# Optimization experiments

Measured on AMD Instinct MI355X. Metric: run time of the kernel, lower is better.

## Reference

```python
import jax, jax.numpy as jnp
import numpy as np

DROPOUT_RATE = 0.6


def dropout(x, key, rate=DROPOUT_RATE):
    keep = jax.random.bernoulli(key, 1.0 - rate, x.shape)
    return jnp.where(keep, x / (1.0 - rate), 0.0).astype(x.dtype)


def gcn_conv(x, W, b, src, dst, n_nodes):
    # h = x @ W  (tiny linear), then symmetric-normalized scatter-add over edges
    h = x @ W                                             # [N, C_out]
    deg = jax.ops.segment_sum(jnp.ones_like(dst, dtype=h.dtype), dst,
                              num_segments=n_nodes)       # in-degree at targets
    dinv = jnp.where(deg > 0, jax.lax.rsqrt(jnp.maximum(deg, 1.0)), 0.0)
    norm = dinv[src] * dinv[dst]                          # [E]
    msg = h[src] * norm[:, None]                          # [E, C_out] gather
    out = jax.ops.segment_sum(msg, dst, num_segments=n_nodes)  # scatter-add
    return out + b


def setup_inputs() -> dict:
    key = jax.random.key(0)
    k_x, k_e, k_w1, k_w2 = jax.random.split(key, 4)
    N, E = 100000, 6400000
    x = jax.random.normal(k_x, (N, 1), dtype=jnp.float32)
    edge_index = jax.random.randint(k_e, (2, E), 0, N, dtype=jnp.int64)
    # GCNConv weights (glorot-ish scale) and zero biases
    W1 = jax.random.normal(k_w1, (1, 16), dtype=jnp.float32) * (1.0 / np.sqrt(1.0))
    b1 = jnp.zeros((16,), dtype=jnp.float32)
    W2 = jax.random.normal(k_w2, (16, 1), dtype=jnp.float32) * (1.0 / np.sqrt(16.0))
    b2 = jnp.zeros((1,), dtype=jnp.float32)
    return {"x": x, "edge_index": edge_index, "W1": W1, "b1": b1, "W2": W2, "b2": b2}


def reference(x, edge_index, W1, b1, W2, b2):
    n_nodes = x.shape[0]
    src, dst = edge_index[0], edge_index[1]
    k1, k2 = jax.random.split(jax.random.key(42), 2)
    h = dropout(x, k1)
    h = gcn_conv(h, W1, b1, src, dst, n_nodes)
    h = jax.nn.relu(h)
    h = dropout(h, k2)
    out = gcn_conv(h, W2, b2, src, dst, n_nodes)
    return out
```

## Files before the change

kernel.cpp:

```cpp
#include <hip/hip_runtime.h>
#include <hip/hip_bf16.h>
#include <stdint.h>


#define KEEP_P 0.4f
#define RANGE 2048
#define SHIFT 11
#define MASK 2047
#define QRANGE 8192
#define QSHIFT 13
#define QMASK 8191
#define BPC 512
#define NCELLMAX 1024
#define TILE 8192
#define TILE4 (TILE / 4)

__host__ __device__ inline unsigned rotl32(unsigned v, int s) {
  return (v << s) | (v >> (32 - s));
}

__host__ __device__ inline void threefry2x32(unsigned key0, unsigned key1,
                                             unsigned x0, unsigned x1,
                                             unsigned& o0, unsigned& o1) {
  unsigned ks0 = key0, ks1 = key1, ks2 = key0 ^ key1 ^ 0x1BD11BDAu;
  unsigned v0 = x0 + ks0, v1 = x1 + ks1;
#define TF_R(r) { v0 += v1; v1 = rotl32(v1, r); v1 ^= v0; }
  TF_R(13) TF_R(15) TF_R(26) TF_R(6)
  v0 += ks1; v1 += ks2 + 1u;
  TF_R(17) TF_R(29) TF_R(16) TF_R(24)
  v0 += ks2; v1 += ks0 + 2u;
  TF_R(13) TF_R(15) TF_R(26) TF_R(6)
  v0 += ks0; v1 += ks1 + 3u;
  TF_R(17) TF_R(29) TF_R(16) TF_R(24)
  v0 += ks1; v1 += ks2 + 4u;
  TF_R(13) TF_R(15) TF_R(26) TF_R(6)
  v0 += ks2; v1 += ks0 + 5u;
#undef TF_R
  o0 = v0; o1 = v1;
}

__device__ inline float u01_from_bits(unsigned bits) {
  return __uint_as_float((bits >> 9) | 0x3f800000u) - 1.0f;
}

__global__ __launch_bounds__(256) void k_cnt(
    const int* __restrict__ src, const int* __restrict__ dst,
    unsigned* __restrict__ counts, int NCELL, int NQ, int e4, int E) {
  __shared__ unsigned cnt[NCELLMAX];
  const int tid = threadIdx.x;
  for (int c = tid; c < NCELL; c += 256) cnt[c] = 0u;
  __syncthreads();
  const int chunk = (e4 + BPC - 1) / BPC;
  const int j0 = blockIdx.x * chunk, j1 = min(j0 + chunk, e4);
  const int4* d4 = reinterpret_cast<const int4*>(dst);
  const int4* s4 = reinterpret_cast<const int4*>(src);
#define CNT1(d, s) atomicAdd(&cnt[((unsigned)(d) >> SHIFT) * NQ + \
                                  ((unsigned)(s) >> QSHIFT)], 1u);
  for (int j = j0 + tid; j < j1; j += 256) {
    int4 d = d4[j]; int4 s = s4[j];
    CNT1(d.x, s.x) CNT1(d.y, s.y) CNT1(d.z, s.z) CNT1(d.w, s.w)
  }
  if (blockIdx.x == 0) {
    for (int t = e4 * 4 + tid; t < E; t += 256) CNT1(dst[t], src[t])
  }
#undef CNT1
  __syncthreads();
  unsigned* my = counts + (size_t)blockIdx.x * NCELL;
  for (int c = tid; c < NCELL; c += 256) my[c] = cnt[c];
}

__global__ __launch_bounds__(256) void k_scan1(
    const unsigned* __restrict__ counts, unsigned* __restrict__ bases,
    unsigned* __restrict__ total, int NCELL) {
  __shared__ unsigned sc[256];
  const int c = blockIdx.x, t = threadIdx.x;
  unsigned c0 = counts[(size_t)(2 * t) * NCELL + c];
  unsigned c1 = counts[(size_t)(2 * t + 1) * NCELL + c];
  unsigned s = c0 + c1;
  sc[t] = s;
  __syncthreads();
  for (int ofs = 1; ofs < 256; ofs <<= 1) {
    unsigned v = (t >= ofs) ? sc[t - ofs] : 0u;
    __syncthreads();
    sc[t] += v;
    __syncthreads();
  }
  unsigned excl = sc[t] - s;
  bases[(size_t)(2 * t) * NCELL + c] = excl;
  bases[(size_t)(2 * t + 1) * NCELL + c] = excl + c0;
  if (t == 255) total[c] = sc[255];
}

__global__ __launch_bounds__(256) void k_scan2(
    const unsigned* __restrict__ total, unsigned* __restrict__ cellstart,
    int NCELL, int E) {
  __shared__ unsigned sc[256];
  const int t = threadIdx.x;
  unsigned l[4]; unsigned s = 0;
  for (int k = 0; k < 4; ++k) {
    int idx = t * 4 + k;
    unsigned v = (idx < NCELL) ? total[idx] : 0u;
    l[k] = s; s += v;
  }
  sc[t] = s;
  __syncthreads();
  for (int ofs = 1; ofs < 256; ofs <<= 1) {
    unsigned v = (t >= ofs) ? sc[t - ofs] : 0u;
    __syncthreads();
    sc[t] += v;
    __syncthreads();
  }
  unsigned excl = sc[t] - s;
  for (int k = 0; k < 4; ++k) {
    int idx = t * 4 + k;
    if (idx < NCELL) cellstart[idx] = excl + l[k];
  }
  if (t == 255) cellstart[NCELL] = (unsigned)E;
}

__global__ __launch_bounds__(256) void k_part(
    const int* __restrict__ src, const int* __restrict__ dst,
    const unsigned* __restrict__ bases, const unsigned* __restrict__ cellstart,
    unsigned* __restrict__ rec, int NCELL, int NQ, int e4, int E) {
  __shared__ unsigned stage[TILE];
  __shared__ unsigned short cellid[TILE];
  __shared__ unsigned hist[NCELLMAX], off[NCELLMAX], tscan[NCELLMAX];
  __shared__ unsigned tbase[NCELLMAX], blkcur[NCELLMAX];
  __shared__ unsigned ssum[256];
  const int tid = threadIdx.x;
  const unsigned* myb = bases + (size_t)blockIdx.x * NCELL;
  for (int c = tid; c < NCELL; c += 256) blkcur[c] = cellstart[c] + myb[c];
  const int chunk = (e4 + BPC - 1) / BPC;
  const int j0 = blockIdx.x * chunk, j1 = min(j0 + chunk, e4);
  const int4* d4 = reinterpret_cast<const int4*>(dst);
  const int4* s4 = reinterpret_cast<const int4*>(src);
  const int K = (NCELL + 255) / 256;

  for (int t0 = j0; t0 < j1; t0 += TILE4) {
    __syncthreads();
    for (int c = tid; c < NCELL; c += 256) hist[c] = 0u;
    __syncthreads();
    const int tcnt = min(TILE4, j1 - t0);
    for (int jj = tid; jj < tcnt; jj += 256) {
      int4 d = d4[t0 + jj]; int4 s = s4[t0 + jj];
      atomicAdd(&hist[((unsigned)d.x >> SHIFT) * NQ + ((unsigned)s.x >> QSHIFT)], 1u);
      atomicAdd(&hist[((unsigned)d.y >> SHIFT) * NQ + ((unsigned)s.y >> QSHIFT)], 1u);
      atomicAdd(&hist[((unsigned)d.z >> SHIFT) * NQ + ((unsigned)s.z >> QSHIFT)], 1u);
      atomicAdd(&hist[((unsigned)d.w >> SHIFT) * NQ + ((unsigned)s.w >> QSHIFT)], 1u);
    }
    __syncthreads();
    unsigned l[4]; unsigned s = 0;
    for (int k = 0; k < K; ++k) {
      int c = tid * K + k;
      unsigned v = (c < NCELL) ? hist[c] : 0u;
      l[k] = s; s += v;
    }
    ssum[tid] = s;
    __syncthreads();
    for (int ofs = 1; ofs < 256; ofs <<= 1) {
      unsigned v = (tid >= ofs) ? ssum[tid - ofs] : 0u;
      __syncthreads();
      ssum[tid] += v;
      __syncthreads();
    }
    unsigned excl = ssum[tid] - s;
    for (int k = 0; k < K; ++k) {
      int c = tid * K + k;
      if (c < NCELL) {
        unsigned e = excl + l[k];
        off[c] = e; tscan[c] = e;
        tbase[c] = blkcur[c];
        blkcur[c] += hist[c];
      }
    }
    __syncthreads();
    for (int jj = tid; jj < tcnt; jj += 256) {
      int4 d = d4[t0 + jj]; int4 s2 = s4[t0 + jj];
#define STG1(dd, ss) { unsigned ud = (unsigned)(dd), us = (unsigned)(ss); \
      unsigned cell = (ud >> SHIFT) * NQ + (us >> QSHIFT); \
      unsigned pos = atomicAdd(&off[cell], 1u); \
      stage[pos] = (ud & MASK) | ((us & QMASK) << SHIFT); \
      cellid[pos] = (unsigned short)cell; }
      STG1(d.x, s2.x) STG1(d.y, s2.y) STG1(d.z, s2.z) STG1(d.w, s2.w)
#undef STG1
    }
    __syncthreads();
    const int tc = 4 * tcnt;
    for (int i = tid; i < tc; i += 256) {
      unsigned c = cellid[i];
      rec[tbase[c] + ((unsigned)i - tscan[c])] = stage[i];
    }
  }
  __syncthreads();
  if (blockIdx.x == 0) {
    for (int t = e4 * 4 + tid; t < E; t += 256) {
      unsigned ud = (unsigned)dst[t], us = (unsigned)src[t];
      unsigned cell = (ud >> SHIFT) * NQ + (us >> QSHIFT);
      unsigned pos = atomicAdd(&blkcur[cell], 1u);
      rec[pos] = (ud & MASK) | ((us & QMASK) << SHIFT);
    }
  }
}

__global__ __launch_bounds__(256) void k_deg(
    const unsigned* __restrict__ rec, const unsigned* __restrict__ cellstart,
    unsigned short* __restrict__ degpart, int NB, int NQ, int SJ) {
  __shared__ unsigned bins[RANGE / 2];
  const int tid = threadIdx.x;
  const int j = blockIdx.x, p = blockIdx.y;
  for (int i = tid; i < RANGE / 2; i += 256) bins[i] = 0u;
  __syncthreads();
  const int s0 = (int)cellstart[p * NQ], s1 = (int)cellstart[(p + 1) * NQ];
  const int len = s1 - s0;
  const int a = s0 + (int)((long)len * j / SJ);
  const int b = s0 + (int)((long)len * (j + 1) / SJ);
#define DEG1(v) { unsigned r = (v) & MASK; \
    atomicAdd(&bins[r >> 1], 1u << ((r & 1) * 16)); }
  int i = a + tid;
  for (; i + 768 < b; i += 1024) {
    unsigned v0 = rec[i], v1 = rec[i + 256], v2 = rec[i + 512], v3 = rec[i + 768];
    DEG1(v0) DEG1(v1) DEG1(v2) DEG1(v3)
  }
  for (; i < b; i += 256) DEG1(rec[i])
#undef DEG1
  __syncthreads();
  unsigned* my32 = (unsigned*)(degpart + ((size_t)j * NB + p) * RANGE);
  for (int i2 = tid; i2 < RANGE / 2; i2 += 256) my32[i2] = bins[i2];
}

__global__ __launch_bounds__(256) void k_node1(
    const float* __restrict__ x, const unsigned short* __restrict__ degpart,
    float* __restrict__ dinv, float* __restrict__ y,
    int NB, int SJ, int n, unsigned k1a, unsigned k1b) {
  int i = blockIdx.x * blockDim.x + threadIdx.x;
  if (i >= n) return;
  const int p = i >> SHIFT, r = i & MASK;
  unsigned d = 0;
  for (int j = 0; j < SJ; ++j) d += degpart[((size_t)j * NB + p) * RANGE + r];
  float di = (d > 0) ? (1.0f / sqrtf((float)d)) : 0.0f;
  dinv[i] = di;
  unsigned o0, o1;
  threefry2x32(k1a, k1b, 0u, (unsigned)i, o0, o1);
  float u = u01_from_bits(o0 ^ o1);
  float xd = (u < KEEP_P) ? (x[i] / KEEP_P) : 0.0f;
  y[i] = xd * di;
}

__global__ __launch_bounds__(256) void k_scat(
    const unsigned* __restrict__ rec, const unsigned* __restrict__ cellstart,
    const float* __restrict__ val, float* __restrict__ part,
    int NB, int NQ, int N) {
  __shared__ float cache[QRANGE];
  __shared__ float bins[RANGE];
  const int tid = threadIdx.x;
  const int q = blockIdx.x, p = blockIdx.y;
  const int g0 = q * QRANGE;
  const int lim = min(QRANGE, N - g0);
  for (int i = tid; i < lim; i += 256) cache[i] = val[g0 + i];
  for (int i = tid; i < RANGE; i += 256) bins[i] = 0.0f;
  __syncthreads();
  const int s0 = (int)cellstart[p * NQ + q], s1 = (int)cellstart[p * NQ + q + 1];
  int i = s0 + tid;
  for (; i + 768 < s1; i += 1024) {
    unsigned v0 = rec[i], v1 = rec[i + 256], v2 = rec[i + 512], v3 = rec[i + 768];
    float f0 = cache[v0 >> SHIFT], f1 = cache[v1 >> SHIFT];
    float f2 = cache[v2 >> SHIFT], f3 = cache[v3 >> SHIFT];
    atomicAdd(&bins[v0 & MASK], f0);
    atomicAdd(&bins[v1 & MASK], f1);
    atomicAdd(&bins[v2 & MASK], f2);
    atomicAdd(&bins[v3 & MASK], f3);
  }
  for (; i < s1; i += 256) {
    unsigned v = rec[i];
    atomicAdd(&bins[v & MASK], cache[v >> SHIFT]);
  }
  __syncthreads();
  float* my = part + ((size_t)q * NB + p) * RANGE;
  for (int i2 = tid; i2 < RANGE; i2 += 256) my[i2] = bins[i2];
}

__global__ __launch_bounds__(256) void k_node2(
    const float* __restrict__ part, const float* __restrict__ dinv,
    const float* __restrict__ W1, const float* __restrict__ b1,
    const float* __restrict__ W2, float* __restrict__ z2,
    int NB, int NQ, int n, unsigned k2a, unsigned k2b) {
  int i = blockIdx.x * blockDim.x + threadIdx.x;
  if (i >= n) return;
  const int p = i >> SHIFT, r = i & MASK;
  float s = 0.0f;
  for (int q = 0; q < NQ; ++q) s += part[((size_t)q * NB + p) * RANGE + r];
  float t = s * dinv[i];
  float z = 0.0f;
  unsigned base = (unsigned)i * 16u;
#pragma unroll
  for (int c = 0; c < 16; ++c) {
    float h = W1[c] * t + b1[c];
    h = fmaxf(h, 0.0f);
    unsigned o0, o1;
    threefry2x32(k2a, k2b, 0u, base + (unsigned)c, o0, o1);
    float u = u01_from_bits(o0 ^ o1);
    float hd = (u < KEEP_P) ? (h / KEEP_P) : 0.0f;
    z += hd * W2[c];
  }
  z2[i] = z * dinv[i];
}

__global__ __launch_bounds__(256) void k_final(
    const float* __restrict__ part, const float* __restrict__ dinv,
    const float* __restrict__ b2, float* __restrict__ out,
    int NB, int NQ, int n) {
  int i = blockIdx.x * blockDim.x + threadIdx.x;
  if (i >= n) return;
  const int p = i >> SHIFT, r = i & MASK;
  float s = 0.0f;
  for (int q = 0; q < NQ; ++q) s += part[((size_t)q * NB + p) * RANGE + r];
  out[i] = b2[0] + dinv[i] * s;
}

extern "C" void kernel_launch(void* const* d_in, const int* in_sizes, int n_in,
                              void* d_out, int out_size, void* d_ws, size_t ws_size,
                              hipStream_t stream) {
  const float* x  = (const float*)d_in[0];
  const int* edge = (const int*)d_in[1];
  const float* W1 = (const float*)d_in[2];
  const float* b1 = (const float*)d_in[3];
  const float* W2 = (const float*)d_in[4];
  const float* b2 = (const float*)d_in[5];
  float* out = (float*)d_out;

  const int N = in_sizes[0];
  const int E = in_sizes[1] / 2;
  const int* src = edge;
  const int* dst = edge + E;

  const int NP = (N + 255) & ~255;
  const int NB = (N + RANGE - 1) / RANGE;
  const int NQ = (N + QRANGE - 1) / QRANGE;
  const int NCELL = NB * NQ;
  const int DSJ = 2 * NQ;

  char* w = (char*)d_ws;
  auto align256 = [](char* p) {
    return (char*)(((uintptr_t)p + 255) & ~(uintptr_t)255);
  };
  unsigned* counts = (unsigned*)w;  w = align256(w + (size_t)BPC * NCELL * 4);
  unsigned* bases  = (unsigned*)w;  w = align256(w + (size_t)BPC * NCELL * 4);
  unsigned* total  = (unsigned*)w;  w = align256(w + (size_t)NCELL * 4);
  unsigned* cellst = (unsigned*)w;  w = align256(w + (size_t)(NCELL + 1) * 4);
  unsigned* rec    = (unsigned*)w;  w = align256(w + (size_t)E * 4);
  float* part_f = (float*)w;
  unsigned short* degpart = (unsigned short*)w;
  size_t part_bytes = (size_t)NQ * NB * RANGE * 4;
  size_t deg_bytes  = (size_t)DSJ * NB * RANGE * 2;
  w = align256(w + (part_bytes > deg_bytes ? part_bytes : deg_bytes));
  float* dinv = (float*)w;
  float* y    = dinv + NP;
  float* z2   = y + NP;

  unsigned k1a, k1b, k2a, k2b;
  threefry2x32(0u, 42u, 0u, 0u, k1a, k1b);
  threefry2x32(0u, 42u, 0u, 1u, k2a, k2b);

  const int e4 = E >> 2;
  const int gN = (N + 255) / 256;

  k_cnt  <<<BPC, 256, 0, stream>>>(src, dst, counts, NCELL, NQ, e4, E);
  k_scan1<<<NCELL, 256, 0, stream>>>(counts, bases, total, NCELL);
  k_scan2<<<1, 256, 0, stream>>>(total, cellst, NCELL, E);
  k_part <<<BPC, 256, 0, stream>>>(src, dst, bases, cellst, rec, NCELL, NQ, e4, E);
  k_deg  <<<dim3(DSJ, NB), 256, 0, stream>>>(rec, cellst, degpart, NB, NQ, DSJ);
  k_node1<<<gN, 256, 0, stream>>>(x, degpart, dinv, y, NB, DSJ, N, k1a, k1b);
  k_scat <<<dim3(NQ, NB), 256, 0, stream>>>(rec, cellst, y, part_f, NB, NQ, N);
  k_node2<<<gN, 256, 0, stream>>>(part_f, dinv, W1, b1, W2, z2, NB, NQ, N, k2a, k2b);
  k_scat <<<dim3(NQ, NB), 256, 0, stream>>>(rec, cellst, z2, part_f, NB, NQ, N);
  k_final<<<gN, 256, 0, stream>>>(part_f, dinv, b2, out, NB, NQ, N);
}
```

Baseline: 260.2 us.

## Decouple count and partition grid sizes, async LDS cache fill, deeper unroll

Splits the single blocks-per-chunk constant into a larger grid for the counting pass and a smaller one for the partition pass, so each partition block takes the combined range of several count blocks. The scan now sums several count entries per thread. The scatter kernel fills its value cache with direct global-to-LDS loads, and both the scatter and degree loops are unrolled to eight loads per iteration for more memory-level parallelism. Costs include a larger counts/bases workspace, longer per-block work in the partition pass, and more register pressure from the wider unroll.

New measurement: 276.2 us. 1.06x slower.

```diff
diff --git a/kernel.cpp b/kernel.cpp
--- a/kernel.cpp
+++ b/kernel.cpp
@@ -10,7 +10,9 @@
 #define QRANGE 8192
 #define QSHIFT 13
 #define QMASK 8191
-#define BPC 512
+#define BPCC 2048
+#define BPCP 256
+#define RATIO (BPCC / BPCP)
 #define NCELLMAX 1024
 #define TILE 8192
 #define TILE4 (TILE / 4)
@@ -50,7 +52,7 @@
   const int tid = threadIdx.x;
   for (int c = tid; c < NCELL; c += 256) cnt[c] = 0u;
   __syncthreads();
-  const int chunk = (e4 + BPC - 1) / BPC;
+  const int chunk = (e4 + BPCC - 1) / BPCC;
   const int j0 = blockIdx.x * chunk, j1 = min(j0 + chunk, e4);
   const int4* d4 = reinterpret_cast<const int4*>(dst);
   const int4* s4 = reinterpret_cast<const int4*>(src);
@@ -74,9 +76,12 @@
     unsigned* __restrict__ total, int NCELL) {
   __shared__ unsigned sc[256];
   const int c = blockIdx.x, t = threadIdx.x;
-  unsigned c0 = counts[(size_t)(2 * t) * NCELL + c];
-  unsigned c1 = counts[(size_t)(2 * t + 1) * NCELL + c];
-  unsigned s = c0 + c1;
+  unsigned l[RATIO];
+  unsigned s = 0;
+  for (int k = 0; k < RATIO; ++k) {
+    unsigned v = counts[(size_t)(t * RATIO + k) * NCELL + c];
+    l[k] = s; s += v;
+  }
   sc[t] = s;
   __syncthreads();
   for (int ofs = 1; ofs < 256; ofs <<= 1) {
@@ -86,8 +91,8 @@
     __syncthreads();
   }
   unsigned excl = sc[t] - s;
-  bases[(size_t)(2 * t) * NCELL + c] = excl;
-  bases[(size_t)(2 * t + 1) * NCELL + c] = excl + c0;
+  for (int k = 0; k < RATIO; ++k)
+    bases[(size_t)(t * RATIO + k) * NCELL + c] = excl + l[k];
   if (t == 255) total[c] = sc[255];
 }
 
@@ -128,9 +133,10 @@
   __shared__ unsigned tbase[NCELLMAX], blkcur[NCELLMAX];
   __shared__ unsigned ssum[256];
   const int tid = threadIdx.x;
-  const unsigned* myb = bases + (size_t)blockIdx.x * NCELL;
+  const unsigned* myb = bases + (size_t)blockIdx.x * RATIO * NCELL;
   for (int c = tid; c < NCELL; c += 256) blkcur[c] = cellstart[c] + myb[c];
-  const int chunk = (e4 + BPC - 1) / BPC;
+  const int chunkC = (e4 + BPCC - 1) / BPCC;
+  const int chunk = RATIO * chunkC;
   const int j0 = blockIdx.x * chunk, j1 = min(j0 + chunk, e4);
   const int4* d4 = reinterpret_cast<const int4*>(dst);
   const int4* s4 = reinterpret_cast<const int4*>(src);
@@ -217,9 +223,12 @@
 #define DEG1(v) { unsigned r = (v) & MASK; \
     atomicAdd(&bins[r >> 1], 1u << ((r & 1) * 16)); }
   int i = a + tid;
-  for (; i + 768 < b; i += 1024) {
-    unsigned v0 = rec[i], v1 = rec[i + 256], v2 = rec[i + 512], v3 = rec[i + 768];
-    DEG1(v0) DEG1(v1) DEG1(v2) DEG1(v3)
+  for (; i + 1792 < b; i += 2048) {
+    unsigned v0 = rec[i],        v1 = rec[i + 256];
+    unsigned v2 = rec[i + 512],  v3 = rec[i + 768];
+    unsigned v4 = rec[i + 1024], v5 = rec[i + 1280];
+    unsigned v6 = rec[i + 1536], v7 = rec[i + 1792];
+    DEG1(v0) DEG1(v1) DEG1(v2) DEG1(v3) DEG1(v4) DEG1(v5) DEG1(v6) DEG1(v7)
   }
   for (; i < b; i += 256) DEG1(rec[i])
 #undef DEG1
@@ -250,25 +259,47 @@
     const unsigned* __restrict__ rec, const unsigned* __restrict__ cellstart,
     const float* __restrict__ val, float* __restrict__ part,
     int NB, int NQ, int N) {
-  __shared__ float cache[QRANGE];
+  __shared__ __align__(16) float cache[QRANGE];
   __shared__ float bins[RANGE];
-  const int tid = threadIdx.x;
+  const int tid = threadIdx.x, w = tid >> 6, lane = tid & 63;
   const int q = blockIdx.x, p = blockIdx.y;
   const int g0 = q * QRANGE;
   const int lim = min(QRANGE, N - g0);
-  for (int i = tid; i < lim; i += 256) cache[i] = val[g0 + i];
+  if (lim == QRANGE) {
+    const float* gsrc = val + g0 + (w << 11) + (lane << 2);
+    float* ldst = cache + (w << 11);
+#pragma unroll
+    for (int k = 0; k < 8; ++k) {
+      __builtin_amdgcn_global_load_lds(
+          (const __attribute__((address_space(1))) void*)(gsrc + (k << 8)),
+          (__attribute__((address_space(3))) void*)(ldst + (k << 8)),
+          16, 0, 0);
+    }
+  } else {
+    for (int i = tid; i < lim; i += 256) cache[i] = val[g0 + i];
+  }
   for (int i = tid; i < RANGE; i += 256) bins[i] = 0.0f;
   __syncthreads();
-  const int s0 = (int)cellstart[p * NQ + q], s1 = (int)cellstart[p * NQ + q + 1];
+  const int s0 = (int)cellstart[p * NQ + q];
+  const int s1 = (int)cellstart[p * NQ + q + 1];
   int i = s0 + tid;
-  for (; i + 768 < s1; i += 1024) {
-    unsigned v0 = rec[i], v1 = rec[i + 256], v2 = rec[i + 512], v3 = rec[i + 768];
+  for (; i + 1792 < s1; i += 2048) {
+    unsigned v0 = rec[i],        v1 = rec[i + 256];
+    unsigned v2 = rec[i + 512],  v3 = rec[i + 768];
+    unsigned v4 = rec[i + 1024], v5 = rec[i + 1280];
+    unsigned v6 = rec[i + 1536], v7 = rec[i + 1792];
     float f0 = cache[v0 >> SHIFT], f1 = cache[v1 >> SHIFT];
     float f2 = cache[v2 >> SHIFT], f3 = cache[v3 >> SHIFT];
+    float f4 = cache[v4 >> SHIFT], f5 = cache[v5 >> SHIFT];
+    float f6 = cache[v6 >> SHIFT], f7 = cache[v7 >> SHIFT];
     atomicAdd(&bins[v0 & MASK], f0);
     atomicAdd(&bins[v1 & MASK], f1);
     atomicAdd(&bins[v2 & MASK], f2);
     atomicAdd(&bins[v3 & MASK], f3);
+    atomicAdd(&bins[v4 & MASK], f4);
+    atomicAdd(&bins[v5 & MASK], f5);
+    atomicAdd(&bins[v6 & MASK], f6);
+    atomicAdd(&bins[v7 & MASK], f7);
   }
   for (; i < s1; i += 256) {
     unsigned v = rec[i];
@@ -343,8 +374,8 @@
   auto align256 = [](char* p) {
     return (char*)(((uintptr_t)p + 255) & ~(uintptr_t)255);
   };
-  unsigned* counts = (unsigned*)w;  w = align256(w + (size_t)BPC * NCELL * 4);
-  unsigned* bases  = (unsigned*)w;  w = align256(w + (size_t)BPC * NCELL * 4);
+  unsigned* counts = (unsigned*)w;  w = align256(w + (size_t)BPCC * NCELL * 4);
+  unsigned* bases  = (unsigned*)w;  w = align256(w + (size_t)BPCC * NCELL * 4);
   unsigned* total  = (unsigned*)w;  w = align256(w + (size_t)NCELL * 4);
   unsigned* cellst = (unsigned*)w;  w = align256(w + (size_t)(NCELL + 1) * 4);
   unsigned* rec    = (unsigned*)w;  w = align256(w + (size_t)E * 4);
@@ -364,10 +395,10 @@
   const int e4 = E >> 2;
   const int gN = (N + 255) / 256;
 
-  k_cnt  <<<BPC, 256, 0, stream>>>(src, dst, counts, NCELL, NQ, e4, E);
+  k_cnt  <<<BPCC, 256, 0, stream>>>(src, dst, counts, NCELL, NQ, e4, E);
   k_scan1<<<NCELL, 256, 0, stream>>>(counts, bases, total, NCELL);
   k_scan2<<<1, 256, 0, stream>>>(total, cellst, NCELL, E);
-  k_part <<<BPC, 256, 0, stream>>>(src, dst, bases, cellst, rec, NCELL, NQ, e4, E);
+  k_part <<<BPCP, 256, 0, stream>>>(src, dst, bases, cellst, rec, NCELL, NQ, e4, E);
   k_deg  <<<dim3(DSJ, NB), 256, 0, stream>>>(rec, cellst, degpart, NB, NQ, DSJ);
   k_node1<<<gN, 256, 0, stream>>>(x, degpart, dinv, y, NB, DSJ, N, k1a, k1b);
   k_scat <<<dim3(NQ, NB), 256, 0, stream>>>(rec, cellst, y, part_f, NB, NQ, N);
```
